# Optimization experiments

Measured on AMD Instinct MI355X. Metric: run time of the kernel, lower is better.

Reference implementation:

```python
import jax, jax.numpy as jnp
import numpy as np

T, B, I, H, NC = 1024, 256, 128, 64, 10


def _lstm_cell(x_t, h, c, W_ih, W_hh, b):
    # PyTorch gate order: i, f, g, o. gates: [B, 4H]
    gates = x_t @ W_ih.T + h @ W_hh.T + b
    i, f, g, o = jnp.split(gates, 4, axis=-1)
    i = jax.nn.sigmoid(i)
    f = jax.nn.sigmoid(f)
    g = jnp.tanh(g)
    o = jax.nn.sigmoid(o)
    c = f * c + i * g
    h = o * jnp.tanh(c)
    return h, c


def setup_inputs() -> dict:
    key = jax.random.key(0)
    ks = jax.random.split(key, 12)
    s = 1.0 / np.sqrt(H)  # PyTorch LSTM init scale
    d = {
        "x": jax.random.normal(ks[0], (T, B, I), dtype=jnp.float32),
        # forward direction LSTM params
        "W_ih_f": jax.random.uniform(ks[1], (4 * H, I), minval=-s, maxval=s, dtype=jnp.float32),
        "W_hh_f": jax.random.uniform(ks[2], (4 * H, H), minval=-s, maxval=s, dtype=jnp.float32),
        "b_f": jax.random.uniform(ks[3], (4 * H,), minval=-s, maxval=s, dtype=jnp.float32),
        # reverse direction LSTM params
        "W_ih_r": jax.random.uniform(ks[4], (4 * H, I), minval=-s, maxval=s, dtype=jnp.float32),
        "W_hh_r": jax.random.uniform(ks[5], (4 * H, H), minval=-s, maxval=s, dtype=jnp.float32),
        "b_r": jax.random.uniform(ks[6], (4 * H,), minval=-s, maxval=s, dtype=jnp.float32),
        # MLP head: 2H -> 64 -> 32 -> NC
        "fc1_w": jax.random.normal(ks[7], (64, 2 * H), dtype=jnp.float32) * 0.05,
        "fc1_b": jnp.zeros((64,), dtype=jnp.float32),
        "fc2_w": jax.random.normal(ks[8], (32, 64), dtype=jnp.float32) * 0.05,
        "fc2_b": jnp.zeros((32,), dtype=jnp.float32),
        "fc3_w": jax.random.normal(ks[9], (NC, 32), dtype=jnp.float32) * 0.05,
        "fc3_b": jnp.zeros((NC,), dtype=jnp.float32),
    }
    return d


def _forward(x, W_ih_f, W_hh_f, b_f, W_ih_r, W_hh_r, b_r,
             fc1_w, fc1_b, fc2_w, fc2_b, fc3_w, fc3_b):
    Bsz = x.shape[1]
    h0 = jnp.zeros((Bsz, H), dtype=x.dtype)
    c0 = jnp.zeros((Bsz, H), dtype=x.dtype)

    # Forward direction: only the final hidden state is needed (output[-1] fwd half).
    def fwd_step(carry, x_t):
        h, c = carry
        h, c = _lstm_cell(x_t, h, c, W_ih_f, W_hh_f, b_f)
        return (h, c), None

    (h_fwd_last, _), _ = jax.lax.scan(fwd_step, (h0, c0), x)

    # Reverse direction: output[-1] reverse half is the hidden after processing
    # x[-1] first (reverse scan starts from the last timestep with zero state).
    h_bwd_last, _ = _lstm_cell(x[-1], h0, c0, W_ih_r, W_hh_r, b_r)

    h_cat = jnp.concatenate([h_fwd_last, h_bwd_last], axis=-1)  # [B, 2H]

    h1 = jax.nn.relu(h_cat @ fc1_w.T + fc1_b)
    h2 = jax.nn.relu(h1 @ fc2_w.T + fc2_b)
    out = h2 @ fc3_w.T + fc3_b  # [B, NC]
    return out


def reference(x, W_ih_f, W_hh_f, b_f, W_ih_r, W_hh_r, b_r,
              fc1_w, fc1_b, fc2_w, fc2_b, fc3_w, fc3_b):
    return _forward(x, W_ih_f, W_hh_f, b_f, W_ih_r, W_hh_r, b_r,
                    fc1_w, fc1_b, fc2_w, fc2_b, fc3_w, fc3_b)
```

## Files before the change

### kernel.cpp

```cpp
#include <hip/hip_runtime.h>
#include <math.h>

#define T_LEN 1024
#define B_SZ  256
#define I_SZ  128
#define H_SZ  64
#define G_SZ  256
#define SUB   32

typedef float f32x8 __attribute__((ext_vector_type(8)));

__device__ __forceinline__ float fast_tanh(float x) {
    float e = __expf(-2.0f * fabsf(x));
    float r = (1.0f - e) * __builtin_amdgcn_rcpf(1.0f + e);
    return copysignf(r, x);
}

#define LD8PIN(V, P)                                                        \
    {   float4 t0_ = *reinterpret_cast<const float4*>(P);                   \
        float4 t1_ = *reinterpret_cast<const float4*>((P) + 4);             \
        V = (f32x8){t0_.x, t0_.y, t0_.z, t0_.w, t1_.x, t1_.y, t1_.z, t1_.w};\
        asm volatile("" : "+v"(V)); }

#define HD(V, M)                                                            \
    {   const float4 ha_ = hp[2*(M)], hb_ = hp[2*(M) + 1];                  \
        a0 = fmaf(ha_.x, V[0], a0); a1 = fmaf(ha_.y, V[1], a1);             \
        a2 = fmaf(ha_.z, V[2], a2); a3 = fmaf(ha_.w, V[3], a3);             \
        a0 = fmaf(hb_.x, V[4], a0); a1 = fmaf(hb_.y, V[5], a1);             \
        a2 = fmaf(hb_.z, V[6], a2); a3 = fmaf(hb_.w, V[7], a3); }

__device__ __forceinline__ int swz(int c) { return c + 4 * (c >> 5); }

__global__ __launch_bounds__(256, 2) void xg_gemm(
    const float* __restrict__ xch,
    const float* __restrict__ W_ih,
    const float* __restrict__ bias,
    float* __restrict__ XG)
{
    const int tid = threadIdx.x;
    const int tx  = tid & 15;
    const int ty  = tid >> 4;
    const int mt  = blockIdx.x;
    const int nt  = blockIdx.y;

    __shared__ __align__(16) float as[32][140];
    __shared__ __align__(16) float bs[32][140];

    const int n0 = nt * 128 + tx * 8;
    float4 bia = *reinterpret_cast<const float4*>(&bias[n0]);
    float4 bib = *reinterpret_cast<const float4*>(&bias[n0 + 4]);

    float acc[8][8];
#pragma unroll
    for (int r = 0; r < 8; ++r)
#pragma unroll
        for (int cc = 0; cc < 8; ++cc) acc[r][cc] = 0.0f;

    const int srow = tid >> 3;
    const int skk  = (tid & 7) * 4;

    for (int ks = 0; ks < 4; ++ks) {
        const int k0 = ks * 32;
        __syncthreads();
#pragma unroll
        for (int i = 0; i < 4; ++i) {
            const int mr = srow + 32 * i;
            float4 xa = *reinterpret_cast<const float4*>(
                &xch[(size_t)(mt * 128 + mr) * I_SZ + k0 + skk]);
            as[skk + 0][swz(mr)] = xa.x; as[skk + 1][swz(mr)] = xa.y;
            as[skk + 2][swz(mr)] = xa.z; as[skk + 3][swz(mr)] = xa.w;
            float4 wa = *reinterpret_cast<const float4*>(
                &W_ih[(size_t)(nt * 128 + mr) * I_SZ + k0 + skk]);
            bs[skk + 0][swz(mr)] = wa.x; bs[skk + 1][swz(mr)] = wa.y;
            bs[skk + 2][swz(mr)] = wa.z; bs[skk + 3][swz(mr)] = wa.w;
        }
        __syncthreads();

#pragma unroll 8
        for (int kk = 0; kk < 32; ++kk) {
            const float4 a0 = *reinterpret_cast<const float4*>(&as[kk][swz(ty * 8)]);
            const float4 a1 = *reinterpret_cast<const float4*>(&as[kk][swz(ty * 8) + 4]);
            const float4 b0 = *reinterpret_cast<const float4*>(&bs[kk][swz(tx * 8)]);
            const float4 b1 = *reinterpret_cast<const float4*>(&bs[kk][swz(tx * 8) + 4]);
            const float av[8] = {a0.x, a0.y, a0.z, a0.w, a1.x, a1.y, a1.z, a1.w};
            const float bv[8] = {b0.x, b0.y, b0.z, b0.w, b1.x, b1.y, b1.z, b1.w};
#pragma unroll
            for (int r = 0; r < 8; ++r)
#pragma unroll
                for (int cc = 0; cc < 8; ++cc)
                    acc[r][cc] = fmaf(av[r], bv[cc], acc[r][cc]);
        }
    }

#pragma unroll
    for (int r = 0; r < 8; ++r) {
        const size_t m = (size_t)(mt * 128 + ty * 8 + r);
        float4 o0 = {acc[r][0] + bia.x, acc[r][1] + bia.y,
                     acc[r][2] + bia.z, acc[r][3] + bia.w};
        float4 o1 = {acc[r][4] + bib.x, acc[r][5] + bib.y,
                     acc[r][6] + bib.z, acc[r][7] + bib.w};
        *reinterpret_cast<float4*>(&XG[m * G_SZ + n0])     = o0;
        *reinterpret_cast<float4*>(&XG[m * G_SZ + n0 + 4]) = o1;
    }
}

__global__ __launch_bounds__(512, 1) void lstm_rec(
    const float* __restrict__ XG,
    const float* __restrict__ W_hh,
    float* __restrict__ h_state,
    float* __restrict__ c_state,
    int TC, int first)
{
    const int b    = blockIdx.x;
    const int t    = threadIdx.x;
    const int half = t & 1;
    const int g    = (t >> 1) & 3;
    const int u    = t >> 3;
    const int row  = (g << 6) | u;

    __shared__ __align__(16) float xgl[2][SUB][G_SZ];
    __shared__ __align__(16) float hsb[2][H_SZ];

    const float* ur = W_hh + row * H_SZ + half * 32;
    f32x8 w0, w1, w2, w3;
    LD8PIN(w0, ur) LD8PIN(w1, ur + 8) LD8PIN(w2, ur + 16) LD8PIN(w3, ur + 24)

    float c = first ? 0.0f : c_state[b * H_SZ + u];
    if (t < H_SZ) hsb[0][t] = first ? 0.0f : h_state[b * H_SZ + t];

    {
        float* xf = &xgl[0][0][0];
#pragma unroll
        for (int i = 0; i < 4; ++i) {
            const int F = t + 512 * i;
            const int r = F >> 6, cw = F & 63;
            *reinterpret_cast<float4*>(xf + 4 * F) =
                *reinterpret_cast<const float4*>(
                    XG + ((size_t)r * B_SZ + b) * G_SZ + 4 * cw);
        }
    }
    __syncthreads();

    const bool isg = (g == 2);
    const int nsub = TC / SUB;
    int pb = 0;
    float hlast = 0.0f;

    for (int sub = 0; sub < nsub; ++sub) {
        const int cur = sub & 1;
        if (sub + 1 < nsub) {
            float* xf = &xgl[cur ^ 1][0][0];
#pragma unroll
            for (int i = 0; i < 4; ++i) {
                const int F = t + 512 * i;
                const int r = (F >> 6) + (sub + 1) * SUB, cw = F & 63;
                *reinterpret_cast<float4*>(xf + 4 * F) =
                    *reinterpret_cast<const float4*>(
                        XG + ((size_t)r * B_SZ + b) * G_SZ + 4 * cw);
            }
        }

#pragma unroll 4
        for (int ts = 0; ts < SUB; ++ts) {
            const float xg = xgl[cur][ts][row];
            const float4* hp =
                reinterpret_cast<const float4*>(&hsb[pb][half * 32]);
            float a0 = 0.0f, a1 = 0.0f, a2 = 0.0f, a3 = 0.0f;
            HD(w0, 0) HD(w1, 1) HD(w2, 2) HD(w3, 3)
            float acc = (a0 + a1) + (a2 + a3);
            acc += __shfl_xor(acc, 1, 64);
            acc += xg;

            const float arg = isg ? (-2.0f * acc) : (-acc);
            const float e = __expf(arg);
            const float r = __builtin_amdgcn_rcpf(1.0f + e);
            const float a = isg ? (1.0f - e) * r : r;

            const float f_ = __shfl_xor(a, 2, 64);
            const float gg = __shfl_xor(a, 4, 64);
            const float o_ = __shfl_xor(f_, 4, 64);

            c = fmaf(f_, c, a * gg);
            hlast = o_ * fast_tanh(c);
            if ((t & 7) == 0) hsb[pb ^ 1][u] = hlast;
            __syncthreads();
            pb ^= 1;
        }
    }

    if ((t & 7) == 0) {
        h_state[b * H_SZ + u] = hlast;
        c_state[b * H_SZ + u] = c;
    }
}

__global__ __launch_bounds__(256, 1) void lstm_tail(
    const float* __restrict__ x_last,
    const float* __restrict__ W_ih_r,
    const float* __restrict__ b_r,
    const float* __restrict__ h_fwd,
    const float* __restrict__ fc1_w,
    const float* __restrict__ fc1_b,
    const float* __restrict__ fc2_w,
    const float* __restrict__ fc2_b,
    const float* __restrict__ fc3_w,
    const float* __restrict__ fc3_b,
    float* __restrict__ out)
{
    const int b = blockIdx.x;
    const int j = threadIdx.x;

    __shared__ float xs[I_SZ];
    __shared__ float gs[G_SZ];
    __shared__ float hc[2 * H_SZ];
    __shared__ float h1[64];
    __shared__ float h2[32];

    if (j < I_SZ) xs[j] = x_last[(size_t)b * I_SZ + j];
    if (j < H_SZ) hc[j] = h_fwd[b * H_SZ + j];
    __syncthreads();

    float a0 = b_r[j], a1 = 0.0f, a2 = 0.0f, a3 = 0.0f;
    const float* wrow = W_ih_r + j * I_SZ;
#pragma unroll
    for (int kk = 0; kk < I_SZ; kk += 4) {
        float4 wv = *reinterpret_cast<const float4*>(wrow + kk);
        a0 = fmaf(xs[kk + 0], wv.x, a0);
        a1 = fmaf(xs[kk + 1], wv.y, a1);
        a2 = fmaf(xs[kk + 2], wv.z, a2);
        a3 = fmaf(xs[kk + 3], wv.w, a3);
    }
    const float acc = (a0 + a1) + (a2 + a3);
    const int gate = j >> 6;
    gs[j] = (gate == 2) ? tanhf(acc) : 1.0f / (1.0f + expf(-acc));
    __syncthreads();

    if (j < H_SZ) {
        const float cc = gs[j] * gs[2 * H_SZ + j];
        hc[H_SZ + j] = gs[3 * H_SZ + j] * tanhf(cc);
    }
    __syncthreads();

    if (j < 64) {
        float s0 = fc1_b[j], s1 = 0.0f, s2 = 0.0f, s3 = 0.0f;
        const float* w = fc1_w + j * 128;
#pragma unroll
        for (int kk = 0; kk < 128; kk += 4) {
            float4 wv = *reinterpret_cast<const float4*>(w + kk);
            s0 = fmaf(hc[kk + 0], wv.x, s0);
            s1 = fmaf(hc[kk + 1], wv.y, s1);
            s2 = fmaf(hc[kk + 2], wv.z, s2);
            s3 = fmaf(hc[kk + 3], wv.w, s3);
        }
        h1[j] = fmaxf((s0 + s1) + (s2 + s3), 0.0f);
    }
    __syncthreads();

    if (j < 32) {
        float s0 = fc2_b[j], s1 = 0.0f, s2 = 0.0f, s3 = 0.0f;
        const float* w = fc2_w + j * 64;
#pragma unroll
        for (int kk = 0; kk < 64; kk += 4) {
            float4 wv = *reinterpret_cast<const float4*>(w + kk);
            s0 = fmaf(h1[kk + 0], wv.x, s0);
            s1 = fmaf(h1[kk + 1], wv.y, s1);
            s2 = fmaf(h1[kk + 2], wv.z, s2);
            s3 = fmaf(h1[kk + 3], wv.w, s3);
        }
        h2[j] = fmaxf((s0 + s1) + (s2 + s3), 0.0f);
    }
    __syncthreads();

    if (j < 10) {
        float s = fc3_b[j];
#pragma unroll
        for (int kk = 0; kk < 32; ++kk) s = fmaf(h2[kk], fc3_w[j * 32 + kk], s);
        out[b * 10 + j] = s;
    }
}

extern "C" void kernel_launch(void* const* d_in, const int* in_sizes, int n_in,
                              void* d_out, int out_size, void* d_ws, size_t ws_size,
                              hipStream_t stream) {
    const float* x      = (const float*)d_in[0];
    const float* W_ih_f = (const float*)d_in[1];
    const float* W_hh_f = (const float*)d_in[2];
    const float* b_f    = (const float*)d_in[3];
    const float* W_ih_r = (const float*)d_in[4];
    const float* b_r    = (const float*)d_in[6];
    const float* fc1_w  = (const float*)d_in[7];
    const float* fc1_b  = (const float*)d_in[8];
    const float* fc2_w  = (const float*)d_in[9];
    const float* fc2_b  = (const float*)d_in[10];
    const float* fc3_w  = (const float*)d_in[11];
    const float* fc3_b  = (const float*)d_in[12];
    float* out = (float*)d_out;

    int TC = 1024;
    while (TC > 64 &&
           (size_t)TC * B_SZ * G_SZ * 4 + 2 * B_SZ * H_SZ * 4 > ws_size)
        TC >>= 1;

    float* XG      = (float*)d_ws;
    float* h_state = (float*)((char*)d_ws + (size_t)TC * B_SZ * G_SZ * 4);
    float* c_state = h_state + B_SZ * H_SZ;

    const int NCH = T_LEN / TC;
    for (int ch = 0; ch < NCH; ++ch) {
        const float* xch = x + (size_t)ch * TC * B_SZ * I_SZ;
        hipLaunchKernelGGL(xg_gemm, dim3(TC * B_SZ / 128, 2), dim3(256), 0,
                           stream, xch, W_ih_f, b_f, XG);
        hipLaunchKernelGGL(lstm_rec, dim3(B_SZ), dim3(512), 0, stream,
                           XG, W_hh_f, h_state, c_state, TC, ch == 0 ? 1 : 0);
    }

    const float* x_last = x + (size_t)(T_LEN - 1) * B_SZ * I_SZ;
    hipLaunchKernelGGL(lstm_tail, dim3(B_SZ), dim3(256), 0, stream,
                       x_last, W_ih_r, b_r, h_state,
                       fc1_w, fc1_b, fc2_w, fc2_b, fc3_w, fc3_b, out);
}
```

Baseline: 744.3 us.

## Exchange LSTM gates through shared memory with per-wave private hidden-state copies

Reworks the recurrent step's thread mapping so each thread pair owns one contiguous gate row. Activated gates are published to a double-buffered shared array, and every wave then redundantly computes the cell update for all 64 units. Each wave keeps its own private copy of h, so the next step's matvec reads wave-local data and needs no second barrier. This replaces the cross-lane shuffle chain with a shared-memory gather, trading extra LDS traffic and redundant elementwise math for a possibly shorter per-step dependency chain.

Measured after the change: 685.8 us. -7.9%, faster.

```diff
diff --git a/kernel.cpp b/kernel.cpp
--- a/kernel.cpp
+++ b/kernel.cpp
@@ -113,20 +113,22 @@
 {
     const int b    = blockIdx.x;
     const int t    = threadIdx.x;
+    const int row  = t >> 1;
     const int half = t & 1;
-    const int g    = (t >> 1) & 3;
-    const int u    = t >> 3;
-    const int row  = (g << 6) | u;
+    const int g    = row >> 6;
+    const int w    = t >> 6;
+    const int l    = t & 63;
 
     __shared__ __align__(16) float xgl[2][SUB][G_SZ];
-    __shared__ __align__(16) float hsb[2][H_SZ];
+    __shared__ __align__(16) float hsb[8][H_SZ];
+    __shared__ float gs[2][G_SZ];
 
     const float* ur = W_hh + row * H_SZ + half * 32;
     f32x8 w0, w1, w2, w3;
     LD8PIN(w0, ur) LD8PIN(w1, ur + 8) LD8PIN(w2, ur + 16) LD8PIN(w3, ur + 24)
 
-    float c = first ? 0.0f : c_state[b * H_SZ + u];
-    if (t < H_SZ) hsb[0][t] = first ? 0.0f : h_state[b * H_SZ + t];
+    float c = first ? 0.0f : c_state[b * H_SZ + l];
+    hsb[w][l] = first ? 0.0f : h_state[b * H_SZ + l];
 
     {
         float* xf = &xgl[0][0][0];
@@ -143,8 +145,8 @@
 
     const bool isg = (g == 2);
     const int nsub = TC / SUB;
-    int pb = 0;
-    float hlast = 0.0f;
+    int db = 0;
+    float h = 0.0f;
 
     for (int sub = 0; sub < nsub; ++sub) {
         const int cur = sub & 1;
@@ -164,7 +166,7 @@
         for (int ts = 0; ts < SUB; ++ts) {
             const float xg = xgl[cur][ts][row];
             const float4* hp =
-                reinterpret_cast<const float4*>(&hsb[pb][half * 32]);
+                reinterpret_cast<const float4*>(&hsb[w][half * 32]);
             float a0 = 0.0f, a1 = 0.0f, a2 = 0.0f, a3 = 0.0f;
             HD(w0, 0) HD(w1, 1) HD(w2, 2) HD(w3, 3)
             float acc = (a0 + a1) + (a2 + a3);
@@ -176,21 +178,23 @@
             const float r = __builtin_amdgcn_rcpf(1.0f + e);
             const float a = isg ? (1.0f - e) * r : r;
 
-            const float f_ = __shfl_xor(a, 2, 64);
-            const float gg = __shfl_xor(a, 4, 64);
-            const float o_ = __shfl_xor(f_, 4, 64);
-
-            c = fmaf(f_, c, a * gg);
-            hlast = o_ * fast_tanh(c);
-            if ((t & 7) == 0) hsb[pb ^ 1][u] = hlast;
+            if (half == 0) gs[db][row] = a;
             __syncthreads();
-            pb ^= 1;
-        }
-    }
-
-    if ((t & 7) == 0) {
-        h_state[b * H_SZ + u] = hlast;
-        c_state[b * H_SZ + u] = c;
+
+            const float ig = gs[db][l];
+            const float fg = gs[db][H_SZ + l];
+            const float gg = gs[db][2 * H_SZ + l];
+            const float og = gs[db][3 * H_SZ + l];
+            c = fmaf(fg, c, ig * gg);
+            h = og * fast_tanh(c);
+            hsb[w][l] = h;
+            db ^= 1;
+        }
+    }
+
+    if (t < H_SZ) {
+        h_state[b * H_SZ + t] = h;
+        c_state[b * H_SZ + t] = c;
     }
 }
 
@@ -245,7 +249,7 @@
         float s0 = fc1_b[j], s1 = 0.0f, s2 = 0.0f, s3 = 0.0f;
         const float* w = fc1_w + j * 128;
 #pragma unroll
-        for (int kk = 0; kk < 128; kk += 4) {
+    for (int kk = 0; kk < 128; kk += 4) {
             float4 wv = *reinterpret_cast<const float4*>(w + kk);
             s0 = fmaf(hc[kk + 0], wv.x, s0);
             s1 = fmaf(hc[kk + 1], wv.y, s1);
```
